# Optimization experiments

Measured on AMD Instinct MI355X. Metric: run time of the kernel, lower is better.

## Reference

```python
import jax, jax.numpy as jnp
import numpy as np

DIM = 768
NUM_HEADS = 12
HEAD_DIM = DIM // NUM_HEADS
H = W = 64
RANK = 4
LORA_SCALING = 1.0 / RANK  # lora_alpha(=1) / r


def setup_inputs() -> dict:
    key = jax.random.key(0)
    ks = jax.random.split(key, 11)
    s = 0.02
    return {
        "x": jax.random.normal(ks[0], (1, H, W, DIM), dtype=jnp.float32),
        "W_qkv": jax.random.normal(ks[1], (3 * DIM, DIM), dtype=jnp.float32) * s,
        "b_qkv": jax.random.normal(ks[2], (3 * DIM,), dtype=jnp.float32) * s,
        "A_q": jax.random.normal(ks[3], (RANK, DIM), dtype=jnp.float32) * s,
        "B_q": jax.random.normal(ks[4], (DIM, RANK), dtype=jnp.float32) * s,
        "A_v": jax.random.normal(ks[5], (RANK, DIM), dtype=jnp.float32) * s,
        "B_v": jax.random.normal(ks[6], (DIM, RANK), dtype=jnp.float32) * s,
        "rel_h": jax.random.normal(ks[7], (2 * H - 1, HEAD_DIM), dtype=jnp.float32) * s,
        "rel_w": jax.random.normal(ks[8], (2 * W - 1, HEAD_DIM), dtype=jnp.float32) * s,
        "W_proj": jax.random.normal(ks[9], (DIM, DIM), dtype=jnp.float32) * s,
        "b_proj": jax.random.normal(ks[10], (DIM,), dtype=jnp.float32) * s,
    }


def _get_rel_pos(size, rel_pos):
    # q_size == k_size == size; relative coords indexed into (2*size-1, head_dim)
    coords = jnp.arange(size)[:, None] - jnp.arange(size)[None, :] + (size - 1)
    return rel_pos[coords]  # (size, size, head_dim)


def reference(x, W_qkv, b_qkv, A_q, B_q, A_v, B_v, rel_h, rel_w, W_proj, b_proj):
    B, h, w, dim = x.shape
    nh, hd = NUM_HEADS, HEAD_DIM
    scale = hd ** -0.5
    n = h * w
    xf = x.reshape(B, n, dim)

    # LoRA-merged QKV: base linear + low-rank deltas on q and v thirds only
    qkv = xf @ W_qkv.T + b_qkv  # (B, n, 3*dim)
    dq = ((xf @ A_q.T) @ B_q.T) * LORA_SCALING
    dv = ((xf @ A_v.T) @ B_v.T) * LORA_SCALING
    qkv = qkv.at[..., :dim].add(dq).at[..., 2 * dim:].add(dv)

    qkv = qkv.reshape(B, n, 3, nh, hd).transpose(2, 0, 3, 1, 4).reshape(3, B * nh, n, hd)
    q, k, v = qkv[0], qkv[1], qkv[2]  # each (B*nh, n, hd)

    attn = (q * scale) @ jnp.swapaxes(k, -2, -1)  # (B*nh, n, n)

    # decomposed relative position bias (SAM style)
    Rh = _get_rel_pos(h, rel_h)  # (h, h, hd)
    Rw = _get_rel_pos(w, rel_w)  # (w, w, hd)
    r_q = q.reshape(B * nh, h, w, hd)
    bias_h = jnp.einsum("bhwc,hkc->bhwk", r_q, Rh)  # (B*nh, h, w, h)
    bias_w = jnp.einsum("bhwc,wkc->bhwk", r_q, Rw)  # (B*nh, h, w, w)
    attn = (attn.reshape(B * nh, h, w, h, w)
            + bias_h[:, :, :, :, None]
            + bias_w[:, :, :, None, :]).reshape(B * nh, n, n)

    attn = jax.nn.softmax(attn, axis=-1)
    out = (attn @ v).reshape(B, nh, h, w, hd).transpose(0, 2, 3, 1, 4).reshape(B, h, w, dim)
    return out @ W_proj.T + b_proj
```

## Files before the change

### kernel.cpp

```cpp
#include <hip/hip_runtime.h>

#define NTOK 4096
#define DIMD 768
#define NHD  12
#define HDD  64
#define DK   800

typedef float  f32x2  __attribute__((ext_vector_type(2)));
typedef float  f32x4  __attribute__((ext_vector_type(4)));
typedef float  f32x16 __attribute__((ext_vector_type(16)));
typedef short  s16x8  __attribute__((ext_vector_type(8)));

#define MFMA16(a, b, c) __builtin_amdgcn_mfma_f32_16x16x32_bf16(a, b, c, 0, 0, 0)
#define MFMA32(a, b, c) __builtin_amdgcn_mfma_f32_32x32x16_bf16(a, b, c, 0, 0, 0)

#if __has_builtin(__builtin_amdgcn_exp2f)
#define EXP2(x) __builtin_amdgcn_exp2f(x)
#else
#define EXP2(x) exp2f(x)
#endif

__device__ inline short f2b(float f) {
  unsigned u = __float_as_uint(f);
  u += 0x7FFFu + ((u >> 16) & 1u);
  return (short)(u >> 16);
}
__device__ inline float b2f(short s) {
  return __uint_as_float(((unsigned)(unsigned short)s) << 16);
}
__device__ inline void gl_lds16(const short* g, short* l) {
  __builtin_amdgcn_global_load_lds(
      (const __attribute__((address_space(1))) unsigned int*)g,
      (__attribute__((address_space(3))) unsigned int*)l, 16, 0, 0);
}


__global__ __launch_bounds__(64)
void k_prep_w(const float* __restrict__ Wqkv, const float* __restrict__ Bq,
              const float* __restrict__ Bv, const float* __restrict__ Wp,
              short* __restrict__ we, short* __restrict__ wpb) {
  const int j = blockIdx.x;
  const int l = threadIdx.x;
  if (j < 2304) {
#pragma unroll
    for (int k = 0; k < 12; ++k)
      we[(size_t)j * DK + l + 64 * k] = f2b(Wqkv[(size_t)j * DIMD + l + 64 * k]);
    if (l < 32) {
      int c = 768 + l;
      short v = 0;
      if (l < 4) {
        if (j < 768) v = f2b(Bq[j * 4 + l]);
      } else if (l < 8) {
        if (j >= 1536) v = f2b(Bv[(j - 1536) * 4 + (l - 4)]);
      }
      we[(size_t)j * DK + c] = v;
    }
  } else {
    const int jr = j - 2304;
#pragma unroll
    for (int k = 0; k < 12; ++k)
      wpb[(size_t)jr * DIMD + l + 64 * k] =
          f2b(Wp[(size_t)jr * DIMD + l + 64 * k]);
  }
}

__global__ __launch_bounds__(64)
void k_prep_x(const float* __restrict__ x, const float* __restrict__ Aq,
              const float* __restrict__ Av, short* __restrict__ xe) {
  const int i = blockIdx.x;
  const int l = threadIdx.x;
  float xv[12];
#pragma unroll
  for (int k = 0; k < 12; ++k) xv[k] = x[(size_t)i * DIMD + l + 64 * k];
#pragma unroll
  for (int k = 0; k < 12; ++k)
    xe[(size_t)i * DK + l + 64 * k] = f2b(xv[k]);
  float a8[8];
#pragma unroll
  for (int o = 0; o < 8; ++o) {
    const float* A = (o < 4) ? (Aq + o * DIMD) : (Av + (o - 4) * DIMD);
    float acc = 0.f;
#pragma unroll
    for (int k = 0; k < 12; ++k) acc = fmaf(xv[k], A[l + 64 * k], acc);
#pragma unroll
    for (int off = 32; off; off >>= 1) acc += __shfl_xor(acc, off, 64);
    a8[o] = acc;
  }
  if (l < 32) {
    float v = 0.f;
#pragma unroll
    for (int o = 0; o < 8; ++o)
      if (l == o) v = 0.25f * a8[o];
    xe[(size_t)i * DK + 768 + l] = (l < 8) ? f2b(v) : (short)0;
  }
}

__global__ __launch_bounds__(256)
void k_qkv(const short* __restrict__ xe, const short* __restrict__ we,
           const float* __restrict__ bqkv, short* __restrict__ qkvb,
           short* __restrict__ vtb) {
  const int d_ = blockIdx.y * 18 + blockIdx.x;
  const int lin = (d_ & 7) * 72 + (d_ >> 3);
  const int j0 = (lin % 18) * 128;
  const int i0 = (lin / 18) * 128;

  __shared__ __align__(16) short shm[16640];
  short* As = shm;
  short* Bs = shm + 8192;
  short* Cs = shm;

  const int t = threadIdx.x, lane = t & 63, w = t >> 6;
  const int l15 = lane & 15, quad = lane >> 4;
  const int wm = w >> 1, wn = w & 1;

  f32x4 acc[4][4];
#pragma unroll
  for (int a = 0; a < 4; ++a)
#pragma unroll
    for (int b = 0; b < 4; ++b) acc[a][b] = (f32x4){0.f, 0.f, 0.f, 0.f};

  for (int kk = 0; kk < 768; kk += 64) {
    __syncthreads();
#pragma unroll
    for (int rep = 0; rep < 4; ++rep) {
      int c = rep * 256 + w * 64 + lane;
      int row = c >> 3, u = (c & 7) ^ (row & 7);
      gl_lds16(xe + (size_t)(i0 + row) * DK + kk + u * 8,
               &As[(rep * 256 + w * 64) * 8]);
      gl_lds16(we + (size_t)(j0 + row) * DK + kk + u * 8,
               &Bs[(rep * 256 + w * 64) * 8]);
    }
    __syncthreads();
#pragma unroll
    for (int kh2 = 0; kh2 < 2; ++kh2) {
      s16x8 af[4], bf[4];
#pragma unroll
      for (int mt = 0; mt < 4; ++mt) {
        int row = wm * 64 + mt * 16 + l15;
        af[mt] = *(const s16x8*)&As[row * 64 +
                                    (((kh2 * 4 + quad) ^ (l15 & 7)) * 8)];
      }
#pragma unroll
      for (int nt = 0; nt < 4; ++nt) {
        int row = wn * 64 + nt * 16 + l15;
        bf[nt] = *(const s16x8*)&Bs[row * 64 +
                                    (((kh2 * 4 + quad) ^ (l15 & 7)) * 8)];
      }
#pragma unroll
      for (int mt = 0; mt < 4; ++mt)
#pragma unroll
        for (int nt = 0; nt < 4; ++nt)
          acc[mt][nt] = MFMA16(af[mt], bf[nt], acc[mt][nt]);
    }
  }

  __syncthreads();
#pragma unroll
  for (int rep = 0; rep < 2; ++rep) {
    int c = rep * 256 + w * 64 + lane;
    gl_lds16(xe + (size_t)(i0 + (c >> 2)) * DK + 768 + (c & 3) * 8,
             &As[(rep * 256 + w * 64) * 8]);
    gl_lds16(we + (size_t)(j0 + (c >> 2)) * DK + 768 + (c & 3) * 8,
             &Bs[(rep * 256 + w * 64) * 8]);
  }
  __syncthreads();
  {
    s16x8 af[4], bf[4];
#pragma unroll
    for (int mt = 0; mt < 4; ++mt)
      af[mt] = *(const s16x8*)&As[(wm * 64 + mt * 16 + l15) * 32 + quad * 8];
#pragma unroll
    for (int nt = 0; nt < 4; ++nt)
      bf[nt] = *(const s16x8*)&Bs[(wn * 64 + nt * 16 + l15) * 32 + quad * 8];
#pragma unroll
    for (int mt = 0; mt < 4; ++mt)
#pragma unroll
      for (int nt = 0; nt < 4; ++nt)
        acc[mt][nt] = MFMA16(af[mt], bf[nt], acc[mt][nt]);
  }
  __syncthreads();

  const int which = j0 / DIMD;
  float bj[4];
#pragma unroll
  for (int nt = 0; nt < 4; ++nt) bj[nt] = bqkv[j0 + wn * 64 + nt * 16 + l15];

#pragma unroll
  for (int mt = 0; mt < 4; ++mt)
#pragma unroll
    for (int r = 0; r < 4; ++r) {
      const int row = wm * 64 + mt * 16 + quad * 4 + r;
#pragma unroll
      for (int nt = 0; nt < 4; ++nt) {
        const int col = wn * 64 + nt * 16 + l15;
        Cs[row * 130 + col] = f2b(acc[mt][nt][r] + bj[nt]);
      }
    }
  __syncthreads();
  const int base_head = (j0 - which * DIMD) >> 6;
  if (which != 2) {
#pragma unroll
    for (int rp = 0; rp < 8; ++rp) {
      int f = t + 256 * rp;
      int row = f >> 4, ch = f & 15;
      int head = base_head + (ch >> 3);
      int ddb = (ch & 7) * 8;
      s16x8 v = *(const s16x8*)&Cs[row * 130 + ch * 8];
      *(s16x8*)&qkvb[(((size_t)which * NHD + head) * NTOK + i0 + row) * HDD + ddb] = v;
    }
  } else {
#pragma unroll
    for (int rp = 0; rp < 8; ++rp) {
      int f = t + 256 * rp;
      int dcol = f >> 4, n8 = (f & 15) * 8;
      unsigned wds[4];
#pragma unroll
      for (int m = 0; m < 4; ++m) {
        int s0 = n8 + 2 * m, s1 = s0 + 1;
        int sr0 = (s0 & 0x70) | ((((s0 >> 2) & 3) == 1 ? 2 : ((s0 >> 2) & 3) == 2 ? 1 : ((s0 >> 2) & 3)) << 2) | (s0 & 3);
        int sr1 = (s1 & 0x70) | ((((s1 >> 2) & 3) == 1 ? 2 : ((s1 >> 2) & 3) == 2 ? 1 : ((s1 >> 2) & 3)) << 2) | (s1 & 3);
        unsigned lo = (unsigned short)Cs[sr0 * 130 + dcol];
        unsigned hi = (unsigned short)Cs[sr1 * 130 + dcol];
        wds[m] = lo | (hi << 16);
      }
      short* dst = vtb + ((size_t)(base_head * 64) + dcol) * NTOK + i0 + n8;
      *(int4*)dst = *(int4*)&wds[0];
    }
  }
}

__global__ __launch_bounds__(256)
void k_attn7(const short* __restrict__ qkvb, const short* __restrict__ vtb,
             const float* __restrict__ relh, const float* __restrict__ relw,
             short* __restrict__ attnb) {
  const int d_ = blockIdx.y * 64 + blockIdx.x;
  const int lin = (d_ & 7) * 96 + (d_ >> 3);
  const int head = lin >> 6;
  const int hq = lin & 63;
  const int n0 = hq * 64;

  __shared__ short sm[20480];
  short* smb = sm;

  const short* qg  = qkvb + (size_t)(0 * NHD + head) * NTOK * HDD;
  const short* kg  = qkvb + (size_t)(1 * NHD + head) * NTOK * HDD;
  const short* vtg = vtb + (size_t)head * HDD * NTOK;

  const int t = threadIdx.x;
  const int w = t >> 6, lane = t & 63;
  const int l31 = lane & 31, h = lane >> 5;
  const int kh = w >> 1, qh = w & 1;
  const int q = qh * 32 + l31;

  const int rowp = lane >> 1;
  const int cw = (w * 2 + (lane & 1)) * 8;
  const short* gK0 = kg + (size_t)rowp * HDD + cw;
  const short* gK1 = gK0 + 32 * HDD;
  const short* gV0 = vtg + (size_t)rowp * NTOK + cw;
  const short* gV1 = gV0 + (size_t)32 * NTOK;

  s16x8 qb[4];
#pragma unroll
  for (int s = 0; s < 4; ++s)
    qb[s] = *(const s16x8*)&qg[(size_t)(n0 + q) * HDD + s * 16 + 8 * h];

#pragma unroll
  for (int rp = 0; rp < 4; ++rp) {
    int f = t + 256 * rp;
    int d = f >> 3, c = (f & 7) * 8;
    float4 v0 = make_float4(0, 0, 0, 0), v1 = v0;
    if (d < 127) {
      const float* s_ = relw + (size_t)d * HDD + c;
      v0 = *(const float4*)s_; v1 = *(const float4*)(s_ + 4);
    }
    short4 b0, b1;
    b0.x = f2b(v0.x); b0.y = f2b(v0.y); b0.z = f2b(v0.z); b0.w = f2b(v0.w);
    b1.x = f2b(v1.x); b1.y = f2b(v1.y); b1.z = f2b(v1.z); b1.w = f2b(v1.w);
    *(short4*)&smb[d * 72 + c] = b0;
    *(short4*)&smb[d * 72 + c + 4] = b1;
  }
  __syncthreads();

  f32x16 mc0 = (f32x16)(0.f), mc1 = (f32x16)(0.f);
#pragma unroll
  for (int s = 0; s < 4; ++s) {
    s16x8 a0 = *(const s16x8*)&smb[((kh * 2) * 32 + l31) * 72 + s * 16 + 8 * h];
    s16x8 a1 = *(const s16x8*)&smb[((kh * 2 + 1) * 32 + l31) * 72 + s * 16 + 8 * h];
    mc0 = MFMA32(a0, qb[s], mc0);
    mc1 = MFMA32(a1, qb[s], mc1);
  }
  __syncthreads();
#pragma unroll
  for (int reg = 0; reg < 16; ++reg) {
    int dl = (reg & 3) + 8 * (reg >> 2) + 4 * h;
    smb[(kh * 64 + dl) * 64 + q] = f2b(mc0[reg] * 1.44269504f);
    smb[(kh * 64 + 32 + dl) * 64 + q] = f2b(mc1[reg] * 1.44269504f);
  }
  __syncthreads();

  f32x2 bw2[8];
#pragma unroll
  for (int i = 0; i < 8; ++i)
#pragma unroll
    for (int p = 0; p < 2; ++p) {
      int reg = 2 * i + p;
      int kl64 = kh * 32 + (reg & 3) + 8 * (reg >> 2) + 4 * h;
      int dneed = q - kl64 + 63;
      bw2[i][p] = b2f(smb[dneed * 64 + q]);
    }
  __syncthreads();

#pragma unroll
  for (int rp = 0; rp < 2; ++rp) {
    int f = t + 256 * rp;
    int kt = f >> 3, c = (f & 7) * 8;
    const float* s_ = relh + (size_t)(hq + 63 - kt) * HDD + c;
    float4 v0 = *(const float4*)s_, v1 = *(const float4*)(s_ + 4);
    short4 b0, b1;
    b0.x = f2b(v0.x); b0.y = f2b(v0.y); b0.z = f2b(v0.z); b0.w = f2b(v0.w);
    b1.x = f2b(v1.x); b1.y = f2b(v1.y); b1.z = f2b(v1.z); b1.w = f2b(v1.w);
    *(short4*)&smb[kt * 72 + c] = b0;
    *(short4*)&smb[kt * 72 + c + 4] = b1;
  }
  __syncthreads();

  f32x16 hc = (f32x16)(0.f);
#pragma unroll
  for (int s = 0; s < 4; ++s) {
    s16x8 a = *(const s16x8*)&smb[(kh * 32 + l31) * 72 + s * 16 + 8 * h];
    hc = MFMA32(a, qb[s], hc);
  }
#pragma unroll
  for (int reg = 0; reg < 16; ++reg) {
    int ktl = kh * 32 + (reg & 3) + 8 * (reg >> 2) + 4 * h;
    smb[16384 + ktl * 64 + q] = f2b(hc[reg] * 1.44269504f);
  }
  __syncthreads();

  gl_lds16(gK0, smb + 0 + w * 512);
  gl_lds16(gK1, smb + 2048 + w * 512);
  gl_lds16(gK0 + 4096, smb + 4096 + w * 512);
  gl_lds16(gK1 + 4096, smb + 4096 + 2048 + w * 512);
  gK0 += 8192; gK1 += 8192;
  gl_lds16(gV0, smb + 8192 + w * 512);
  gl_lds16(gV1, smb + 8192 + 2048 + w * 512);
  gl_lds16(gV0 + 64, smb + 12288 + w * 512);
  gl_lds16(gV1 + 64, smb + 12288 + 2048 + w * 512);
  gV0 += 128; gV1 += 128;

  int baseS[4], baseV[2];
#pragma unroll
  for (int s = 0; s < 4; ++s)
    baseS[s] = kh * 2048 + s * 512 + l31 * 16 + h * 8;
#pragma unroll
  for (int s2 = 0; s2 < 2; ++s2)
    baseV[s2] = (kh * 2 + s2) * 512 + l31 * 16 + h * 8;

  f32x2 ps2 = (f32x2)(0.f);
  f32x16 oc0 = (f32x16)(0.f), oc1 = (f32x16)(0.f);

#define SM_BLOCK(SC, BHL, PK)                                                  \
    _Pragma("unroll") for (int i = 0; i < 8; ++i) {                            \
      f32x2 s2;                                                                \
      s2[0] = (SC)[2 * i]; s2[1] = (SC)[2 * i + 1];                            \
      f32x2 r = s2 * 0.18033688f + (bw2[i] + (BHL));                           \
      float e0 = EXP2(r[0]);                                                   \
      float e1 = EXP2(r[1]);                                                   \
      f32x2 e2; e2[0] = e0; e2[1] = e1;                                        \
      ps2 += e2;                                                               \
      PK[i] = __builtin_amdgcn_perm(__float_as_uint(e1),                       \
                                    __float_as_uint(e0), 0x07060302u);         \
    }

#define PV_BLOCK(VOFF, PK)                                                     \
    _Pragma("unroll") for (int s2i = 0; s2i < 2; ++s2i) {                      \
      union { unsigned u[4]; s16x8 v; } B;                                     \
      B.u[0] = PK[4 * s2i + 0]; B.u[1] = PK[4 * s2i + 1];                      \
      B.u[2] = PK[4 * s2i + 2]; B.u[3] = PK[4 * s2i + 3];                      \
      s16x8 a0 = *(const s16x8*)&smb[(VOFF) + baseV[s2i]];                     \
      s16x8 a1 = *(const s16x8*)&smb[(VOFF) + 2048 + baseV[s2i]];              \
      oc0 = MFMA32(a0, B.v, oc0);                                              \
      oc1 = MFMA32(a1, B.v, oc1);                                              \
    }

#define ITER2(KTa, PF)                                                         \
  {                                                                            \
    asm volatile("s_waitcnt vmcnt(4)" ::: "memory");                           \
    __builtin_amdgcn_s_barrier();                                              \
    __builtin_amdgcn_sched_barrier(0);                                         \
    f32x16 sa = (f32x16)(0.f), sb = (f32x16)(0.f);                             \
    _Pragma("unroll") for (int s = 0; s < 4; ++s) {                            \
      s16x8 ka = *(const s16x8*)&smb[0 + baseS[s]];                            \
      sa = MFMA32(ka, qb[s], sa);                                              \
    }                                                                          \
    _Pragma("unroll") for (int s = 0; s < 4; ++s) {                            \
      s16x8 kb = *(const s16x8*)&smb[4096 + baseS[s]];                         \
      sb = MFMA32(kb, qb[s], sb);                                              \
    }                                                                          \
    float bhla = b2f(smb[16384 + (KTa) * 64 + q]);                             \
    float bhlb = b2f(smb[16384 + (KTa) * 64 + 64 + q]);                        \
    asm volatile("s_waitcnt lgkmcnt(0) vmcnt(0)" ::: "memory");                \
    __builtin_amdgcn_sched_barrier(0);                                         \
    __builtin_amdgcn_s_barrier();                                              \
    __builtin_amdgcn_sched_barrier(0);                                         \
    if (PF) {                                                                  \
      gl_lds16(gK0, smb + 0 + w * 512);                                        \
      gl_lds16(gK1, smb + 2048 + w * 512);                                     \
      gl_lds16(gK0 + 4096, smb + 4096 + w * 512);                              \
      gl_lds16(gK1 + 4096, smb + 4096 + 2048 + w * 512);                       \
      gK0 += 8192; gK1 += 8192;                                                \
    }                                                                          \
    unsigned pkA[8], pkB[8];                                                   \
    SM_BLOCK(sa, bhla, pkA);                                                   \
    PV_BLOCK(8192, pkA);                                                       \
    SM_BLOCK(sb, bhlb, pkB);                                                   \
    PV_BLOCK(12288, pkB);                                                      \
    if (PF) {                                                                  \
      asm volatile("s_waitcnt lgkmcnt(0)" ::: "memory");                       \
      __builtin_amdgcn_sched_barrier(0);                                       \
      __builtin_amdgcn_s_barrier();                                            \
      __builtin_amdgcn_sched_barrier(0);                                       \
      gl_lds16(gV0, smb + 8192 + w * 512);                                     \
      gl_lds16(gV1, smb + 8192 + 2048 + w * 512);                              \
      gl_lds16(gV0 + 64, smb + 12288 + w * 512);                               \
      gl_lds16(gV1 + 64, smb + 12288 + 2048 + w * 512);                        \
      gV0 += 128; gV1 += 128;                                                  \
    }                                                                          \
  }

  for (int t2 = 0; t2 < 31; ++t2) {
    ITER2(2 * t2, 1);
  }
  ITER2(62, 0);
#undef ITER2
#undef SM_BLOCK
#undef PV_BLOCK

  __syncthreads();
  float ps = ps2[0] + ps2[1];
  float* obuf = (float*)smb;
  float* psb  = (float*)smb + 4224;
  short* tbuf = smb + 8576;
  ps += __shfl_xor(ps, 32, 64);
  if (kh == 1) {
#pragma unroll
    for (int reg = 0; reg < 16; ++reg) {
      int dl = (reg & 3) + 8 * (reg >> 2) + 4 * h;
      obuf[dl * 66 + q] = oc0[reg];
      obuf[(32 + dl) * 66 + q] = oc1[reg];
    }
    if (lane < 32) psb[q] = ps;
  }
  __syncthreads();
  if (kh == 0) {
    float inv = 1.f / (ps + psb[q]);
#pragma unroll
    for (int reg = 0; reg < 16; ++reg) {
      int dl = (reg & 3) + 8 * (reg >> 2) + 4 * h;
      tbuf[dl * 66 + q] = f2b((oc0[reg] + obuf[dl * 66 + q]) * inv);
      tbuf[(32 + dl) * 66 + q] = f2b((oc1[reg] + obuf[(32 + dl) * 66 + q]) * inv);
    }
  }
  __syncthreads();
  {
    int qq = t >> 2, seg = t & 3;
    unsigned wds[8];
#pragma unroll
    for (int m = 0; m < 8; ++m) {
      unsigned lo = (unsigned short)tbuf[(seg * 16 + 2 * m) * 66 + qq];
      unsigned hi = (unsigned short)tbuf[(seg * 16 + 2 * m + 1) * 66 + qq];
      wds[m] = lo | (hi << 16);
    }
    short* dst = attnb + (size_t)(n0 + qq) * DIMD + head * 64 + seg * 16;
    *(int4*)dst = *(int4*)&wds[0];
    *(int4*)(dst + 8) = *(int4*)&wds[4];
  }
}

__global__ __launch_bounds__(256)
void k_proj(const short* __restrict__ ab, const short* __restrict__ wpb,
            const float* __restrict__ bp, float* __restrict__ out) {
  const int d_ = blockIdx.y * 12 + blockIdx.x;
  const int lin = (d_ & 7) * 48 + (d_ >> 3);
  const int j0 = (lin % 12) * 64;
  const int i0 = (lin / 12) * 128;
  __shared__ short As[128 * 32];
  __shared__ short Bs[64 * 32];
  const int t = threadIdx.x, lane = t & 63, w = t >> 6;
  const int l15 = lane & 15, quad = lane >> 4;
  const int wm = w >> 1, wn = w & 1;

  f32x4 acc[4][2];
#pragma unroll
  for (int a = 0; a < 4; ++a)
#pragma unroll
    for (int b = 0; b < 2; ++b) acc[a][b] = (f32x4){0.f, 0.f, 0.f, 0.f};

  for (int kk = 0; kk < DIMD; kk += 32) {
    __syncthreads();
#pragma unroll
    for (int rep = 0; rep < 2; ++rep) {
      int c = rep * 256 + w * 64 + lane;
      gl_lds16(ab + (size_t)(i0 + (c >> 2)) * DIMD + kk + (c & 3) * 8,
               &As[(rep * 256 + w * 64) * 8]);
    }
    {
      gl_lds16(wpb + (size_t)(j0 + ((w * 64 + lane) >> 2)) * DIMD + kk +
                   ((w * 64 + lane) & 3) * 8,
               &Bs[(w * 64) * 8]);
    }
    __syncthreads();
    s16x8 af[4], bf[2];
#pragma unroll
    for (int mt = 0; mt < 4; ++mt)
      af[mt] = *(const s16x8*)&As[(wm * 64 + mt * 16 + l15) * 32 + quad * 8];
#pragma unroll
    for (int nt = 0; nt < 2; ++nt)
      bf[nt] = *(const s16x8*)&Bs[(wn * 32 + nt * 16 + l15) * 32 + quad * 8];
#pragma unroll
    for (int mt = 0; mt < 4; ++mt)
#pragma unroll
      for (int nt = 0; nt < 2; ++nt)
        acc[mt][nt] = MFMA16(af[mt], bf[nt], acc[mt][nt]);
  }

#pragma unroll
  for (int mt = 0; mt < 4; ++mt)
#pragma unroll
    for (int r = 0; r < 4; ++r) {
      const int i = i0 + wm * 64 + mt * 16 + quad * 4 + r;
#pragma unroll
      for (int nt = 0; nt < 2; ++nt) {
        const int j = j0 + wn * 32 + nt * 16 + l15;
        out[(size_t)i * DIMD + j] = acc[mt][nt][r] + bp[j];
      }
    }
}

extern "C" void kernel_launch(void* const* d_in, const int* in_sizes, int n_in,
                              void* d_out, int out_size, void* d_ws, size_t ws_size,
                              hipStream_t stream) {
  (void)in_sizes; (void)n_in; (void)out_size; (void)ws_size;
  const float* x    = (const float*)d_in[0];
  const float* Wqkv = (const float*)d_in[1];
  const float* bqkv = (const float*)d_in[2];
  const float* Aq   = (const float*)d_in[3];
  const float* Bq   = (const float*)d_in[4];
  const float* Av   = (const float*)d_in[5];
  const float* Bv   = (const float*)d_in[6];
  const float* relh = (const float*)d_in[7];
  const float* relw = (const float*)d_in[8];
  const float* Wp   = (const float*)d_in[9];
  const float* bp   = (const float*)d_in[10];
  float* out = (float*)d_out;

  float* ws = (float*)d_ws;
  short* xe    = (short*)(ws);
  short* we    = (short*)(ws + 1638400);
  short* wpb   = (short*)(ws + 2560000);
  short* qkvb  = (short*)(ws + 2854912);
  short* vtb   = (short*)(ws + 7573504);
  short* attnb = (short*)(ws + 9146368);

  k_prep_w<<<dim3(3072), dim3(64), 0, stream>>>(Wqkv, Bq, Bv, Wp, we, wpb);
  k_prep_x<<<dim3(NTOK), dim3(64), 0, stream>>>(x, Aq, Av, xe);
  k_qkv<<<dim3(18, 32), dim3(256), 0, stream>>>(xe, we, bqkv, qkvb, vtb);
  k_attn7<<<dim3(64, NHD), dim3(256), 0, stream>>>(qkvb, vtb, relh, relw, attnb);
  k_proj<<<dim3(12, 32), dim3(256), 0, stream>>>(attnb, wpb, bp, out);
}
```

Before: 222.1 us.

## Split attention over four key chunks and merge partial outputs in a combine kernel

The attention kernel now splits each (head, query-tile) block into four key-range quarters, giving four times as many workgroups to fill the GPU. Each quarter writes a normalized fp16 partial output plus its softmax denominator to scratch buffers that reuse dead workspace regions. A new k_comb kernel merges the four partials with the denominators as weights and writes the bf16 attention output. The cost is an extra launch, extra global traffic for the partials, and fp16 rounding of the intermediate results.

```diff
diff --git a/kernel.cpp b/kernel.cpp
--- a/kernel.cpp
+++ b/kernel.cpp
@@ -232,14 +232,18 @@
 __global__ __launch_bounds__(256)
 void k_attn7(const short* __restrict__ qkvb, const short* __restrict__ vtb,
              const float* __restrict__ relh, const float* __restrict__ relw,
-             short* __restrict__ attnb) {
-  const int d_ = blockIdx.y * 64 + blockIdx.x;
-  const int lin = (d_ & 7) * 96 + (d_ >> 3);
-  const int head = lin >> 6;
-  const int hq = lin & 63;
+             short* __restrict__ p0, short* __restrict__ p1,
+             short* __restrict__ p2, short* __restrict__ p3,
+             float* __restrict__ psv) {
+  const int d_ = blockIdx.y * 256 + blockIdx.x;
+  const int lin = (d_ & 7) * 384 + (d_ >> 3);
+  const int quarter = lin & 3;
+  const int lin4 = lin >> 2;
+  const int head = lin4 >> 6;
+  const int hq = lin4 & 63;
   const int n0 = hq * 64;
 
-  __shared__ short sm[20480];
+  __shared__ short sm[17408];
   short* smb = sm;
 
   const short* qg  = qkvb + (size_t)(0 * NHD + head) * NTOK * HDD;
@@ -254,9 +258,9 @@
 
   const int rowp = lane >> 1;
   const int cw = (w * 2 + (lane & 1)) * 8;
-  const short* gK0 = kg + (size_t)rowp * HDD + cw;
+  const short* gK0 = kg + (size_t)quarter * 1024 * HDD + (size_t)rowp * HDD + cw;
   const short* gK1 = gK0 + 32 * HDD;
-  const short* gV0 = vtg + (size_t)rowp * NTOK + cw;
+  const short* gV0 = vtg + (size_t)rowp * NTOK + cw + quarter * 1024;
   const short* gV1 = gV0 + (size_t)32 * NTOK;
 
   s16x8 qb[4];
@@ -310,30 +314,31 @@
     }
   __syncthreads();
 
-#pragma unroll
-  for (int rp = 0; rp < 2; ++rp) {
-    int f = t + 256 * rp;
-    int kt = f >> 3, c = (f & 7) * 8;
-    const float* s_ = relh + (size_t)(hq + 63 - kt) * HDD + c;
-    float4 v0 = *(const float4*)s_, v1 = *(const float4*)(s_ + 4);
+  {
+    int ktl = t >> 3, c = (t & 7) * 8;
+    float4 v0 = make_float4(0, 0, 0, 0), v1 = v0;
+    if (ktl < 16) {
+      const float* s_ = relh + (size_t)(hq + 63 - (quarter * 16 + ktl)) * HDD + c;
+      v0 = *(const float4*)s_; v1 = *(const float4*)(s_ + 4);
+    }
     short4 b0, b1;
     b0.x = f2b(v0.x); b0.y = f2b(v0.y); b0.z = f2b(v0.z); b0.w = f2b(v0.w);
     b1.x = f2b(v1.x); b1.y = f2b(v1.y); b1.z = f2b(v1.z); b1.w = f2b(v1.w);
-    *(short4*)&smb[kt * 72 + c] = b0;
-    *(short4*)&smb[kt * 72 + c + 4] = b1;
+    *(short4*)&smb[ktl * 72 + c] = b0;
+    *(short4*)&smb[ktl * 72 + c + 4] = b1;
   }
   __syncthreads();
 
   f32x16 hc = (f32x16)(0.f);
 #pragma unroll
   for (int s = 0; s < 4; ++s) {
-    s16x8 a = *(const s16x8*)&smb[(kh * 32 + l31) * 72 + s * 16 + 8 * h];
+    s16x8 a = *(const s16x8*)&smb[l31 * 72 + s * 16 + 8 * h];
     hc = MFMA32(a, qb[s], hc);
   }
 #pragma unroll
   for (int reg = 0; reg < 16; ++reg) {
-    int ktl = kh * 32 + (reg & 3) + 8 * (reg >> 2) + 4 * h;
-    smb[16384 + ktl * 64 + q] = f2b(hc[reg] * 1.44269504f);
+    int ktl = (reg & 3) + 8 * (reg >> 2) + 4 * h;
+    if (ktl < 16) smb[16384 + ktl * 64 + q] = f2b(hc[reg] * 1.44269504f);
   }
   __syncthreads();
 
@@ -428,10 +433,10 @@
     }                                                                          \
   }
 
-  for (int t2 = 0; t2 < 31; ++t2) {
+  for (int t2 = 0; t2 < 7; ++t2) {
     ITER2(2 * t2, 1);
   }
-  ITER2(62, 0);
+  ITER2(14, 0);
 #undef ITER2
 #undef SM_BLOCK
 #undef PV_BLOCK
@@ -453,28 +458,80 @@
   }
   __syncthreads();
   if (kh == 0) {
-    float inv = 1.f / (ps + psb[q]);
+    float denom = ps + psb[q];
+    float inv = 1.f / denom;
 #pragma unroll
     for (int reg = 0; reg < 16; ++reg) {
       int dl = (reg & 3) + 8 * (reg >> 2) + 4 * h;
-      tbuf[dl * 66 + q] = f2b((oc0[reg] + obuf[dl * 66 + q]) * inv);
-      tbuf[(32 + dl) * 66 + q] = f2b((oc1[reg] + obuf[(32 + dl) * 66 + q]) * inv);
-    }
+      union { _Float16 hh; short s; } u0, u1;
+      u0.hh = (_Float16)((oc0[reg] + obuf[dl * 66 + q]) * inv);
+      u1.hh = (_Float16)((oc1[reg] + obuf[(32 + dl) * 66 + q]) * inv);
+      tbuf[dl * 66 + q] = u0.s;
+      tbuf[(32 + dl) * 66 + q] = u1.s;
+    }
+    if (lane < 32) psv[((size_t)lin4 * 4 + quarter) * 64 + q] = denom;
   }
   __syncthreads();
   {
+    short* pdst = (quarter == 0) ? p0 : (quarter == 1) ? p1
+                  : (quarter == 2) ? p2 : p3;
+    pdst += (size_t)lin4 * 4096;
     int qq = t >> 2, seg = t & 3;
     unsigned wds[8];
 #pragma unroll
     for (int m = 0; m < 8; ++m) {
-      unsigned lo = (unsigned short)tbuf[(seg * 16 + 2 * m) * 66 + qq];
-      unsigned hi = (unsigned short)tbuf[(seg * 16 + 2 * m + 1) * 66 + qq];
+      unsigned lo = (unsigned short)tbuf[qq * 66 + seg * 16 + 2 * m];
+      unsigned hi = (unsigned short)tbuf[qq * 66 + seg * 16 + 2 * m + 1];
+      lo = (unsigned short)tbuf[(seg * 16 + 2 * m) * 66 + qq];
+      hi = (unsigned short)tbuf[(seg * 16 + 2 * m + 1) * 66 + qq];
       wds[m] = lo | (hi << 16);
     }
-    short* dst = attnb + (size_t)(n0 + qq) * DIMD + head * 64 + seg * 16;
+    short* dst = pdst + qq * 64 + seg * 16;
     *(int4*)dst = *(int4*)&wds[0];
     *(int4*)(dst + 8) = *(int4*)&wds[4];
   }
+}
+
+__global__ __launch_bounds__(256)
+void k_comb(const short* __restrict__ p0, const short* __restrict__ p1,
+            const short* __restrict__ p2, const short* __restrict__ p3,
+            const float* __restrict__ psv, short* __restrict__ attnb) {
+  const int lin4 = blockIdx.x;
+  const int head = lin4 >> 6, hq = lin4 & 63, n0 = hq * 64;
+  const int t = threadIdx.x;
+  const int q = t >> 2, seg = t & 3, d0 = seg * 16;
+  float acc[16];
+#pragma unroll
+  for (int i = 0; i < 16; ++i) acc[i] = 0.f;
+  float W = 0.f;
+#pragma unroll
+  for (int c = 0; c < 4; ++c) {
+    const short* pc = (c == 0) ? p0 : (c == 1) ? p1 : (c == 2) ? p2 : p3;
+    float wc = psv[((size_t)lin4 * 4 + c) * 64 + q];
+    W += wc;
+    const short* src = pc + (size_t)lin4 * 4096 + q * 64 + d0;
+    union { int4 v; short s[8]; } A, B;
+    A.v = *(const int4*)src;
+    B.v = *(const int4*)(src + 8);
+#pragma unroll
+    for (int i = 0; i < 8; ++i) {
+      union { short s; _Float16 hh; } ua, ub;
+      ua.s = A.s[i]; ub.s = B.s[i];
+      acc[i]     += (float)ua.hh * wc;
+      acc[8 + i] += (float)ub.hh * wc;
+    }
+  }
+  float inv = 1.f / W;
+  unsigned wds[8];
+#pragma unroll
+  for (int m = 0; m < 8; ++m) {
+    unsigned lo = (unsigned short)f2b(acc[2 * m] * inv);
+    unsigned hi = (unsigned short)f2b(acc[2 * m + 1] * inv);
+    wds[m] = lo | (hi << 16);
+  }
+  short* dst = attnb + (size_t)(n0 + q) * DIMD + head * 64 + d0;
+  *(int4*)dst = *(int4*)&wds[0];
+  *(int4*)(dst + 8) = *(int4*)&wds[4];
 }
 
 __global__ __launch_bounds__(256)
@@ -562,9 +619,18 @@
   short* vtb   = (short*)(ws + 7573504);
   short* attnb = (short*)(ws + 9146368);
 
+  short* shws = (short*)ws;
+  short* pb0 = shws;
+  short* pb1 = shws + 12001280;
+  short* pb2 = shws + 21438464;
+  short* pb3 = shws + 24584192;
+  float* psv = ws + 1638400;
+
   k_prep_w<<<dim3(3072), dim3(64), 0, stream>>>(Wqkv, Bq, Bv, Wp, we, wpb);
   k_prep_x<<<dim3(NTOK), dim3(64), 0, stream>>>(x, Aq, Av, xe);
   k_qkv<<<dim3(18, 32), dim3(256), 0, stream>>>(xe, we, bqkv, qkvb, vtb);
-  k_attn7<<<dim3(64, NHD), dim3(256), 0, stream>>>(qkvb, vtb, relh, relw, attnb);
+  k_attn7<<<dim3(256, NHD), dim3(256), 0, stream>>>(qkvb, vtb, relh, relw,
+                                                    pb0, pb1, pb2, pb3, psv);
+  k_comb<<<dim3(768), dim3(256), 0, stream>>>(pb0, pb1, pb2, pb3, psv, attnb);
   k_proj<<<dim3(12, 32), dim3(256), 0, stream>>>(attnb, wpb, bp, out);
 }
```

After: 232.2 us. +4.5%, slower.

## Load K/V tiles directly into registers with double-buffering instead of LDS staging

Applied to the files above, without the earlier changes.

Replaces the LDS-staged K and V^T pipeline (global-to-LDS async loads, barriers, LDS reads) with direct per-lane global loads into register fragments, double-buffered across tiles. This removes the block-wide barriers and LDS traffic inside the main attention loop. In exchange each wave now fetches its own K/V fragments from global memory or cache, with less coalesced, possibly redundant loads across waves, and uses more registers, which could lower occupancy or expose memory latency.

```diff
diff --git a/kernel.cpp b/kernel.cpp
--- a/kernel.cpp
+++ b/kernel.cpp
@@ -252,12 +252,9 @@
   const int kh = w >> 1, qh = w & 1;
   const int q = qh * 32 + l31;
 
-  const int rowp = lane >> 1;
-  const int cw = (w * 2 + (lane & 1)) * 8;
-  const short* gK0 = kg + (size_t)rowp * HDD + cw;
-  const short* gK1 = gK0 + 32 * HDD;
-  const short* gV0 = vtg + (size_t)rowp * NTOK + cw;
-  const short* gV1 = gV0 + (size_t)32 * NTOK;
+  const short* kbase  = kg + (size_t)(kh * 32 + l31) * HDD + h * 8;
+  const short* vbase0 = vtg + (size_t)l31 * NTOK + (kh * 4 + h) * 8;
+  const short* vbase1 = vbase0 + (size_t)32 * NTOK;
 
   s16x8 qb[4];
 #pragma unroll
@@ -337,104 +334,60 @@
   }
   __syncthreads();
 
-  gl_lds16(gK0, smb + 0 + w * 512);
-  gl_lds16(gK1, smb + 2048 + w * 512);
-  gl_lds16(gK0 + 4096, smb + 4096 + w * 512);
-  gl_lds16(gK1 + 4096, smb + 4096 + 2048 + w * 512);
-  gK0 += 8192; gK1 += 8192;
-  gl_lds16(gV0, smb + 8192 + w * 512);
-  gl_lds16(gV1, smb + 8192 + 2048 + w * 512);
-  gl_lds16(gV0 + 64, smb + 12288 + w * 512);
-  gl_lds16(gV1 + 64, smb + 12288 + 2048 + w * 512);
-  gV0 += 128; gV1 += 128;
-
-  int baseS[4], baseV[2];
-#pragma unroll
-  for (int s = 0; s < 4; ++s)
-    baseS[s] = kh * 2048 + s * 512 + l31 * 16 + h * 8;
-#pragma unroll
-  for (int s2 = 0; s2 < 2; ++s2)
-    baseV[s2] = (kh * 2 + s2) * 512 + l31 * 16 + h * 8;
-
   f32x2 ps2 = (f32x2)(0.f);
   f32x16 oc0 = (f32x16)(0.f), oc1 = (f32x16)(0.f);
 
-#define SM_BLOCK(SC, BHL, PK)                                                  \
+#define LOADK(DST, KT)                                                         \
+  _Pragma("unroll") for (int s = 0; s < 4; ++s)                                \
+    DST[s] = *(const s16x8*)&kbase[(size_t)(KT) * 4096 + s * 16];
+
+#define LOADV(DST, KT)                                                         \
+  _Pragma("unroll") for (int s2 = 0; s2 < 2; ++s2) {                           \
+    DST[s2]     = *(const s16x8*)&vbase0[(size_t)(KT) * 64 + s2 * 16];         \
+    DST[2 + s2] = *(const s16x8*)&vbase1[(size_t)(KT) * 64 + s2 * 16];         \
+  }
+
+#define TILE(KT, KF, VF)                                                       \
+  {                                                                            \
+    f32x16 sc_ = (f32x16)(0.f);                                                \
+    _Pragma("unroll") for (int s = 0; s < 4; ++s)                              \
+      sc_ = MFMA32(KF[s], qb[s], sc_);                                         \
+    float bhl2 = b2f(smb[16384 + (KT) * 64 + q]);                              \
+    unsigned pk[8];                                                            \
     _Pragma("unroll") for (int i = 0; i < 8; ++i) {                            \
       f32x2 s2;                                                                \
-      s2[0] = (SC)[2 * i]; s2[1] = (SC)[2 * i + 1];                            \
-      f32x2 r = s2 * 0.18033688f + (bw2[i] + (BHL));                           \
+      s2[0] = sc_[2 * i]; s2[1] = sc_[2 * i + 1];                              \
+      f32x2 r = s2 * 0.18033688f + (bw2[i] + bhl2);                            \
       float e0 = EXP2(r[0]);                                                   \
       float e1 = EXP2(r[1]);                                                   \
       f32x2 e2; e2[0] = e0; e2[1] = e1;                                        \
       ps2 += e2;                                                               \
-      PK[i] = __builtin_amdgcn_perm(__float_as_uint(e1),                       \
+      pk[i] = __builtin_amdgcn_perm(__float_as_uint(e1),                       \
                                     __float_as_uint(e0), 0x07060302u);         \
-    }
-
-#define PV_BLOCK(VOFF, PK)                                                     \
+    }                                                                          \
     _Pragma("unroll") for (int s2i = 0; s2i < 2; ++s2i) {                      \
       union { unsigned u[4]; s16x8 v; } B;                                     \
-      B.u[0] = PK[4 * s2i + 0]; B.u[1] = PK[4 * s2i + 1];                      \
-      B.u[2] = PK[4 * s2i + 2]; B.u[3] = PK[4 * s2i + 3];                      \
-      s16x8 a0 = *(const s16x8*)&smb[(VOFF) + baseV[s2i]];                     \
-      s16x8 a1 = *(const s16x8*)&smb[(VOFF) + 2048 + baseV[s2i]];              \
-      oc0 = MFMA32(a0, B.v, oc0);                                              \
-      oc1 = MFMA32(a1, B.v, oc1);                                              \
-    }
-
-#define ITER2(KTa, PF)                                                         \
-  {                                                                            \
-    asm volatile("s_waitcnt vmcnt(4)" ::: "memory");                           \
-    __builtin_amdgcn_s_barrier();                                              \
-    __builtin_amdgcn_sched_barrier(0);                                         \
-    f32x16 sa = (f32x16)(0.f), sb = (f32x16)(0.f);                             \
-    _Pragma("unroll") for (int s = 0; s < 4; ++s) {                            \
-      s16x8 ka = *(const s16x8*)&smb[0 + baseS[s]];                            \
-      sa = MFMA32(ka, qb[s], sa);                                              \
+      B.u[0] = pk[4 * s2i + 0]; B.u[1] = pk[4 * s2i + 1];                      \
+      B.u[2] = pk[4 * s2i + 2]; B.u[3] = pk[4 * s2i + 3];                      \
+      oc0 = MFMA32(VF[s2i], B.v, oc0);                                         \
+      oc1 = MFMA32(VF[2 + s2i], B.v, oc1);                                     \
     }                                                                          \
-    _Pragma("unroll") for (int s = 0; s < 4; ++s) {                            \
-      s16x8 kb = *(const s16x8*)&smb[4096 + baseS[s]];                         \
-      sb = MFMA32(kb, qb[s], sb);                                              \
-    }                                                                          \
-    float bhla = b2f(smb[16384 + (KTa) * 64 + q]);                             \
-    float bhlb = b2f(smb[16384 + (KTa) * 64 + 64 + q]);                        \
-    asm volatile("s_waitcnt lgkmcnt(0) vmcnt(0)" ::: "memory");                \
-    __builtin_amdgcn_sched_barrier(0);                                         \
-    __builtin_amdgcn_s_barrier();                                              \
-    __builtin_amdgcn_sched_barrier(0);                                         \
-    if (PF) {                                                                  \
-      gl_lds16(gK0, smb + 0 + w * 512);                                        \
-      gl_lds16(gK1, smb + 2048 + w * 512);                                     \
-      gl_lds16(gK0 + 4096, smb + 4096 + w * 512);                              \
-      gl_lds16(gK1 + 4096, smb + 4096 + 2048 + w * 512);                       \
-      gK0 += 8192; gK1 += 8192;                                                \
-    }                                                                          \
-    unsigned pkA[8], pkB[8];                                                   \
-    SM_BLOCK(sa, bhla, pkA);                                                   \
-    PV_BLOCK(8192, pkA);                                                       \
-    SM_BLOCK(sb, bhlb, pkB);                                                   \
-    PV_BLOCK(12288, pkB);                                                      \
-    if (PF) {                                                                  \
-      asm volatile("s_waitcnt lgkmcnt(0)" ::: "memory");                       \
-      __builtin_amdgcn_sched_barrier(0);                                       \
-      __builtin_amdgcn_s_barrier();                                            \
-      __builtin_amdgcn_sched_barrier(0);                                       \
-      gl_lds16(gV0, smb + 8192 + w * 512);                                     \
-      gl_lds16(gV1, smb + 8192 + 2048 + w * 512);                              \
-      gl_lds16(gV0 + 64, smb + 12288 + w * 512);                               \
-      gl_lds16(gV1 + 64, smb + 12288 + 2048 + w * 512);                        \
-      gV0 += 128; gV1 += 128;                                                  \
-    }                                                                          \
-  }
-
+  }
+
+  s16x8 kA[4], vA[4], kB[4], vB[4];
+  LOADK(kA, 0); LOADV(vA, 0);
   for (int t2 = 0; t2 < 31; ++t2) {
-    ITER2(2 * t2, 1);
-  }
-  ITER2(62, 0);
-#undef ITER2
-#undef SM_BLOCK
-#undef PV_BLOCK
+    LOADK(kB, 2 * t2 + 1); LOADV(vB, 2 * t2 + 1);
+    TILE(2 * t2, kA, vA);
+    LOADK(kA, 2 * t2 + 2); LOADV(vA, 2 * t2 + 2);
+    TILE(2 * t2 + 1, kB, vB);
+  }
+  LOADK(kB, 63); LOADV(vB, 63);
+  TILE(62, kA, vA);
+  TILE(63, kB, vB);
+#undef TILE
+#undef LOADK
+#undef LOADV
 
   __syncthreads();
   float ps = ps2[0] + ps2[1];
```

Result: slower. 306.4 us (+38.0%).
